# Kernel optimization log

Hardware: AMD Instinct MI355X
Metric: run time of the kernel (lower is better)

## Reference

```python
import jax, jax.numpy as jnp
import numpy as np

B, T, C, U = 64, 250, 1024, 512


def setup_inputs() -> dict:
    key = jax.random.key(0)
    ks = jax.random.split(key, 9)
    inputs = jax.random.normal(ks[0], (B, T, C), dtype=jnp.float32)
    # contiguous padding mask: True for valid positions
    seq_len = jax.random.randint(ks[1], (B,), T // 2, T + 1)
    mask = jnp.arange(T)[None, :] < seq_len[:, None]
    s_in = 1.0 / np.sqrt(C)
    s_rec = 1.0 / np.sqrt(U)
    Wf = jax.random.normal(ks[2], (C, 3 * U), dtype=jnp.float32) * s_in
    Uf = jax.random.normal(ks[3], (U, 3 * U), dtype=jnp.float32) * s_rec
    bf = jnp.zeros((2, 3 * U), dtype=jnp.float32)  # [input_bias, recurrent_bias] (reset_after=True)
    Wb = jax.random.normal(ks[4], (C, 3 * U), dtype=jnp.float32) * s_in
    Ub = jax.random.normal(ks[5], (U, 3 * U), dtype=jnp.float32) * s_rec
    bb = jnp.zeros((2, 3 * U), dtype=jnp.float32)
    return {"inputs": inputs, "mask": mask, "Wf": Wf, "Uf": Uf, "bf": bf,
            "Wb": Wb, "Ub": Ub, "bb": bb}


def _gru(x_tbc, m_tb, W, Uk, b):
    """Keras GRU v2 (reset_after=True) with masking. x_tbc: [T,B,C], m_tb: [T,B]."""
    # precompute input projections for all timesteps: [T,B,3U]
    xg = jnp.einsum('tbc,cg->tbg', x_tbc, W) + b[0]

    def step(h, inp):
        xg_t, m_t = inp
        hg = h @ Uk + b[1]  # [B,3U]
        xz, xr, xh = jnp.split(xg_t, 3, axis=-1)
        hz, hr, hh = jnp.split(hg, 3, axis=-1)
        z = jax.nn.sigmoid(xz + hz)
        r = jax.nn.sigmoid(xr + hr)
        c = jnp.tanh(xh + r * hh)
        h_new = z * h + (1.0 - z) * c
        h_new = jnp.where(m_t[:, None], h_new, h)  # carry state through masked steps
        return h_new, h_new

    h0 = jnp.zeros((x_tbc.shape[1], Uk.shape[0]), x_tbc.dtype)
    hT, ys = jax.lax.scan(step, h0, (xg, m_tb))
    return ys, hT  # ys: [T,B,U], hT: [B,U]


def reference(inputs, mask, Wf, Uf, bf, Wb, Ub, bb):
    x_t = jnp.transpose(inputs, (1, 0, 2))  # [T,B,C]
    m_t = mask.T  # [T,B]
    y_f, h_f = _gru(x_t, m_t, Wf, Uf, bf)
    # go_backwards: process reversed sequence, then reverse outputs back
    y_b, h_b = _gru(x_t[::-1], m_t[::-1], Wb, Ub, bb)
    y_b = y_b[::-1]
    seq_out = jnp.transpose(jnp.concatenate([y_f, y_b], axis=-1), (1, 0, 2))  # [B,T,2U]
    state_out = jnp.concatenate([h_f, h_b], axis=-1)  # [B,2U]
    return seq_out, state_out
```

## Files before the change

### kernel.cpp

```cpp
#include <hip/hip_runtime.h>
#include <cmath>

#define BB 64
#define TT 250
#define CC 1024
#define GG 1536

typedef unsigned long long u64t;
typedef unsigned int uint32;
typedef unsigned short ushort16;
typedef __attribute__((ext_vector_type(8))) short short8v;
typedef __attribute__((ext_vector_type(4))) float f32x4;

#define O_XGF 0
#define O_XGB 24576000
#define O_UT  49152000
#define O_MF  50724864
#define O_VH  50740864
#define O_WT  51003008

__device__ __forceinline__ unsigned short f2bf(float f) {
  unsigned u = __float_as_uint(f);
  return (unsigned short)((u + 0x7fffu + ((u >> 16) & 1u)) >> 16);
}
__device__ __forceinline__ float bf2f(unsigned short h) {
  return __uint_as_float((unsigned)h << 16);
}
__device__ __forceinline__ void cvt2(float a, float b, uint32& hi, uint32& lo) {
  unsigned short ha = f2bf(a), hb = f2bf(b);
  hi = (uint32)ha | ((uint32)hb << 16);
  lo = (uint32)f2bf(a - bf2f(ha)) | ((uint32)f2bf(b - bf2f(hb)) << 16);
}

__global__ __launch_bounds__(256) void prep_kernel(
    const unsigned char* __restrict__ mraw,
    float* __restrict__ ut, float* __restrict__ mf, u64t* __restrict__ vh,
    const float* __restrict__ Uf, const float* __restrict__ Ub)
{
  int idx = blockIdx.x * 256 + threadIdx.x;
  if (idx < 2*512*3*512) {
    int k = idx & 511;
    int r = idx >> 9;
    int g = r % 3;
    int rest = r / 3;
    int u = rest & 511;
    int dd = rest >> 9;
    const float* Um = dd ? Ub : Uf;
    ut[idx] = Um[k*GG + (g << 9) + u];
  }
  if (idx < 131072)
    __hip_atomic_store(&vh[idx], 0ULL, __ATOMIC_RELAXED, __HIP_MEMORY_SCOPE_AGENT);
  if (idx < BB*TT) {
    int b = idx / TT, t = idx - b*TT;
    bool bytefmt = (mraw[1] == 1);
    bool mv = bytefmt ? (mraw[idx] != 0) : (((const int*)mraw)[idx] != 0);
    mf[t*BB + b] = mv ? 1.0f : 0.0f;
  }
}

__global__ __launch_bounds__(256) void wt_build(
    const float* __restrict__ Wf, const float* __restrict__ Wb,
    ushort16* __restrict__ wt_hi, ushort16* __restrict__ wt_lo)
{
  __shared__ float tile[64][65];
  const int k0 = blockIdx.x * 64;
  const int n0 = blockIdx.y * 64;
  const int d  = blockIdx.z;
  const float* W = d ? Wb : Wf;
  const int l = threadIdx.x & 63, w = threadIdx.x >> 6;
  #pragma unroll
  for (int j = 0; j < 16; j++) {
    int r = j*4 + w;
    tile[r][l] = W[(size_t)(k0+r)*GG + n0 + l];
  }
  __syncthreads();
  #pragma unroll
  for (int j = 0; j < 16; j++) {
    int r = j*4 + w;
    float f = tile[l][r];
    unsigned short h = f2bf(f);
    size_t o = (size_t)(d*GG + n0 + r)*1024 + k0 + l;
    wt_hi[o] = h;
    wt_lo[o] = f2bf(f - bf2f(h));
  }
}

#define LDFRAG(dst, arr, row, kg) do { \
    union { uint4 u; short8v s; } r_; \
    r_.u = *(const uint4*)&arr[(row)*40 + ((kg) << 3)]; \
    dst = r_.s; } while (0)

__global__ __launch_bounds__(256) void gemm_xg(
    const float* __restrict__ A,
    const ushort16* __restrict__ wt_hi, const ushort16* __restrict__ wt_lo,
    const float* __restrict__ bf, const float* __restrict__ bb,
    float* __restrict__ xgf, float* __restrict__ xgb)
{
  __shared__ __align__(16) ushort16 Ah[128*40];
  __shared__ __align__(16) ushort16 Al[128*40];
  __shared__ __align__(16) ushort16 Bh[128*40];
  __shared__ __align__(16) ushort16 Bl[128*40];
  const int tid = threadIdx.x;
  const int l  = tid & 63;
  const int wv = tid >> 6;
  const int wm = wv & 1;
  const int wn = wv >> 1;
  const int t0 = blockIdx.x * 2;
  const int n0 = blockIdx.y * 128;
  const int d  = (n0 >= GG) ? 1 : 0;
  const int nl0 = n0 - d*GG;
  const float* bias = d ? bb : bf;
  float* xg = d ? xgb : xgf;

  const int sr = tid >> 1;
  const int sk = (tid & 1) << 4;
  const ushort16* whp = wt_hi + (size_t)(d*GG + nl0 + sr)*1024 + sk;
  const ushort16* wlp = wt_lo + (size_t)(d*GG + nl0 + sr)*1024 + sk;
  const int mrow = (sr & 63)*TT + t0 + (sr >> 6);
  const float* xp = A + (size_t)mrow*CC + sk;

  f32x4 acc[4][4];
  #pragma unroll
  for (int i = 0; i < 4; i++)
    #pragma unroll
    for (int j = 0; j < 4; j++) acc[i][j] = (f32x4){0.f,0.f,0.f,0.f};

  const int kg = l >> 4;
  for (int k0 = 0; k0 < CC; k0 += 32) {
    uint4 ha = *(const uint4*)(whp + k0);
    uint4 hb = *(const uint4*)(whp + k0 + 8);
    uint4 la = *(const uint4*)(wlp + k0);
    uint4 lb = *(const uint4*)(wlp + k0 + 8);
    float4 x0 = *(const float4*)(xp + k0);
    float4 x1 = *(const float4*)(xp + k0 + 4);
    float4 x2 = *(const float4*)(xp + k0 + 8);
    float4 x3 = *(const float4*)(xp + k0 + 12);
    __syncthreads();
    {
      *(uint4*)&Ah[sr*40 + sk]     = ha;
      *(uint4*)&Ah[sr*40 + sk + 8] = hb;
      *(uint4*)&Al[sr*40 + sk]     = la;
      *(uint4*)&Al[sr*40 + sk + 8] = lb;
      uint32 bhv[8], blv[8];
      cvt2(x0.x, x0.y, bhv[0], blv[0]); cvt2(x0.z, x0.w, bhv[1], blv[1]);
      cvt2(x1.x, x1.y, bhv[2], blv[2]); cvt2(x1.z, x1.w, bhv[3], blv[3]);
      cvt2(x2.x, x2.y, bhv[4], blv[4]); cvt2(x2.z, x2.w, bhv[5], blv[5]);
      cvt2(x3.x, x3.y, bhv[6], blv[6]); cvt2(x3.z, x3.w, bhv[7], blv[7]);
      *(uint4*)&Bh[sr*40 + sk]     = make_uint4(bhv[0], bhv[1], bhv[2], bhv[3]);
      *(uint4*)&Bh[sr*40 + sk + 8] = make_uint4(bhv[4], bhv[5], bhv[6], bhv[7]);
      *(uint4*)&Bl[sr*40 + sk]     = make_uint4(blv[0], blv[1], blv[2], blv[3]);
      *(uint4*)&Bl[sr*40 + sk + 8] = make_uint4(blv[4], blv[5], blv[6], blv[7]);
    }
    __syncthreads();
    short8v afh[4], afl[4], bfh[4], bfl[4];
    #pragma unroll
    for (int i = 0; i < 4; i++) {
      const int rA = wn*64 + i*16 + (l & 15);
      LDFRAG(afh[i], Ah, rA, kg);
      LDFRAG(afl[i], Al, rA, kg);
      const int rB = wm*64 + i*16 + (l & 15);
      LDFRAG(bfh[i], Bh, rB, kg);
      LDFRAG(bfl[i], Bl, rB, kg);
    }
    #pragma unroll
    for (int i = 0; i < 4; i++)
      #pragma unroll
      for (int j = 0; j < 4; j++) {
        acc[i][j] = __builtin_amdgcn_mfma_f32_16x16x32_bf16(afh[i], bfh[j], acc[i][j], 0, 0, 0);
        acc[i][j] = __builtin_amdgcn_mfma_f32_16x16x32_bf16(afh[i], bfl[j], acc[i][j], 0, 0, 0);
        acc[i][j] = __builtin_amdgcn_mfma_f32_16x16x32_bf16(afl[i], bfh[j], acc[i][j], 0, 0, 0);
      }
  }
  const int t = t0 + wm;
  #pragma unroll
  for (int i = 0; i < 4; i++) {
    const int ugl = wn*64 + i*16 + ((l >> 4) << 2);
    #pragma unroll
    for (int r = 0; r < 4; r++) {
      const int n = nl0 + ugl + r;
      const float bv = bias[n];
      float* orow = xg + (size_t)t*98304 + ((size_t)(n >> 9) << 15) + ((n & 511) << 6);
      #pragma unroll
      for (int j = 0; j < 4; j++)
        orow[j*16 + (l & 15)] = acc[i][j][r] + bv;
    }
  }
}

__global__ __launch_bounds__(512, 2) void gru_scan(
    float* xgf, float* xgb,
    const float* __restrict__ ut, const float* __restrict__ bf,
    const float* __restrict__ bb, const float* __restrict__ mf,
    u64t* vh, float* __restrict__ out)
{
  __shared__ __align__(16) unsigned short Bhi[8192];
  __shared__ __align__(16) unsigned short Blo[8192];
  const int tid = threadIdx.x;
  const int l   = tid & 63;
  const int wv  = tid >> 6;
  const int bid = blockIdx.x;
  const int d     = bid >> 6;
  const int mb    = (bid >> 2) & 15;
  const int btile = bid & 3;

  short8v af_hi[16], af_lo[16];
  {
    const int row = (wv << 4) | (l & 15);
    const int g   = row & 3;
    const int ua  = (mb << 5) | (row >> 2);
    const int kg_ = (l >> 4) << 3;
    if (g < 3) {
      const float* ap = ut + (((size_t)(((d << 9) | ua) * 3 + g)) << 9);
      #pragma unroll
      for (int ks = 0; ks < 16; ks++) {
        #pragma unroll
        for (int j = 0; j < 8; j++) {
          float f = ap[(ks << 5) + kg_ + j];
          unsigned short h = f2bf(f);
          af_hi[ks][j] = (short)h;
          af_lo[ks][j] = (short)f2bf(f - bf2f(h));
        }
      }
    } else {
      #pragma unroll
      for (int ks = 0; ks < 16; ks++)
        #pragma unroll
        for (int j = 0; j < 8; j++) { af_hi[ks][j] = 0; af_lo[ks][j] = 0; }
    }
  }

  const int u  = (mb << 5) | (wv << 2) | (l >> 4);
  const int b  = (btile << 4) | (l & 15);
  const float* bias = (d ? bb : bf) + GG;
  const float b1z = bias[u], b1r = bias[512+u], b1h = bias[1024+u];
  float* xg = d ? xgb : xgf;
  float hprev = 0.0f;

  const int kc  = tid >> 4;
  const int blw = tid & 15;
  const int cb  = (btile << 4) | blw;
  const int ksub_w = kc >> 1;
  const int qbase  = (kc & 1) << 1;
  const int boff = ((l & 15) << 6) + (((l >> 4) ^ ((l >> 1) & 3)) << 4);

  const int tf = d ? (TT-1) : 0;
  const float* xp0 = xg + (size_t)tf*98304 + (u << 6) + b;
  float xz = xp0[0], xr = xp0[32768], xh = xp0[65536];
  float m = mf[tf*BB + b];

  for (int s = 0; s < TT; s++) {
    const unsigned us_ = (unsigned)s;
    const int t = d ? (TT-1-s) : s;
    u64t* vin = vh + (size_t)((((unsigned)s & 1u) << 1) | (unsigned)d) * 32768;

    u64t v[16];
    #pragma unroll
    for (int i = 0; i < 16; i++)
      v[i] = __hip_atomic_load(vin + ((kc << 4) + i)*64 + cb, __ATOMIC_RELAXED, __HIP_MEMORY_SCOPE_AGENT);
    while (true) {
      int bad = 0;
      #pragma unroll
      for (int i = 0; i < 16; i++) bad |= ((unsigned)(v[i] >> 32) < us_) ? 1 : 0;
      if (!__any(bad)) break;
      __builtin_amdgcn_s_sleep(1);
      #pragma unroll
      for (int i = 0; i < 16; i++)
        if ((unsigned)(v[i] >> 32) < us_)
          v[i] = __hip_atomic_load(vin + ((kc << 4) + i)*64 + cb, __ATOMIC_RELAXED, __HIP_MEMORY_SCOPE_AGENT);
    }

    __syncthreads();
    #pragma unroll
    for (int half = 0; half < 2; half++) {
      uint32 hw[4], lw[4];
      #pragma unroll
      for (int p = 0; p < 4; p++) {
        u64t v0 = v[(half << 3) + (p << 1)];
        u64t v1 = v[(half << 3) + (p << 1) + 1];
        hw[p] = (uint32)((v0 >> 16) & 0xffffu) | ((uint32)((v1 >> 16) & 0xffffu) << 16);
        lw[p] = (uint32)(v0 & 0xffffu)         | ((uint32)(v1 & 0xffffu) << 16);
      }
      const int phys = (qbase + half) ^ ((blw >> 1) & 3);
      const int off = (ksub_w << 10) + (blw << 6) + (phys << 4);
      *(uint4*)((char*)Bhi + off) = make_uint4(hw[0], hw[1], hw[2], hw[3]);
      *(uint4*)((char*)Blo + off) = make_uint4(lw[0], lw[1], lw[2], lw[3]);
    }
    __syncthreads();

    float xz_n = 0.f, xr_n = 0.f, xh_n = 0.f, m_n = 0.f;
    if (s+1 < TT) {
      const int t2 = d ? (TT-2-s) : (s+1);
      const float* xp = xg + (size_t)t2*98304 + (u << 6) + b;
      xz_n = xp[0]; xr_n = xp[32768]; xh_n = xp[65536];
      m_n  = mf[t2*BB + b];
    }

    f32x4 acc0 = {0.f,0.f,0.f,0.f};
    f32x4 acc1 = {0.f,0.f,0.f,0.f};
    f32x4 acc2 = {0.f,0.f,0.f,0.f};
    #pragma unroll
    for (int ks = 0; ks < 16; ks++) {
      short8v bh  = *(const short8v*)((const char*)Bhi + (ks << 10) + boff);
      short8v bl8 = *(const short8v*)((const char*)Blo + (ks << 10) + boff);
      acc0 = __builtin_amdgcn_mfma_f32_16x16x32_bf16(af_hi[ks], bh,  acc0, 0, 0, 0);
      acc1 = __builtin_amdgcn_mfma_f32_16x16x32_bf16(af_hi[ks], bl8, acc1, 0, 0, 0);
      acc2 = __builtin_amdgcn_mfma_f32_16x16x32_bf16(af_lo[ks], bh,  acc2, 0, 0, 0);
    }
    float az = acc0[0] + acc1[0] + acc2[0];
    float ar = acc0[1] + acc1[1] + acc2[1];
    float ah = acc0[2] + acc1[2] + acc2[2];

    float z  = 1.0f / (1.0f + expf(-(xz + az + b1z)));
    float r  = 1.0f / (1.0f + expf(-(xr + ar + b1r)));
    float cc = tanhf(xh + r * (ah + b1h));
    float hn = z*hprev + (1.0f - z)*cc;
    hn = (m != 0.0f) ? hn : hprev;
    hprev = hn;

    u64t* vout = vh + (size_t)(((((unsigned)s + 1u) & 1u) << 1) | (unsigned)d) * 32768;
    unsigned short hh = f2bf(hn);
    unsigned short hl = f2bf(hn - bf2f(hh));
    u64t pk = ((u64t)(unsigned)(s+1) << 32) | ((u64t)hh << 16) | (u64t)hl;
    __hip_atomic_store(&vout[(u << 6) | b], pk, __ATOMIC_RELAXED, __HIP_MEMORY_SCOPE_AGENT);
    xg[(size_t)t*98304 + ((size_t)u << 6) + b] = hn;
    xz = xz_n; xr = xr_n; xh = xh_n; m = m_n;
  }
  out[16384000ull + ((size_t)b << 10) + (d << 9) + u] = hprev;
}

__global__ __launch_bounds__(256) void y_transpose(
    const float* __restrict__ xgf, const float* __restrict__ xgb,
    float* __restrict__ out)
{
  __shared__ float tile[64][65];
  const int t  = blockIdx.x;
  const int ch = blockIdx.y;
  const int d  = ch >> 3, uc = ch & 7;
  const float* src = (d ? xgb : xgf) + (size_t)t*98304 + (size_t)uc*4096;
  const int lane = threadIdx.x & 63, w = threadIdx.x >> 6;
  #pragma unroll
  for (int j = 0; j < 16; j++) {
    int r = j*4 + w;
    tile[r][lane] = src[r*64 + lane];
  }
  __syncthreads();
  #pragma unroll
  for (int j = 0; j < 16; j++) {
    int b = j*4 + w;
    out[((size_t)b*TT + t)*1024 + (d << 9) + (uc << 6) + lane] = tile[lane][b];
  }
}

extern "C" void kernel_launch(void* const* d_in, const int* in_sizes, int n_in,
                              void* d_out, int out_size, void* d_ws, size_t ws_size,
                              hipStream_t stream) {
  const float* X  = (const float*)d_in[0];
  const unsigned char* Mk = (const unsigned char*)d_in[1];
  const float* Wf = (const float*)d_in[2];
  const float* Uf = (const float*)d_in[3];
  const float* bf = (const float*)d_in[4];
  const float* Wb = (const float*)d_in[5];
  const float* Ub = (const float*)d_in[6];
  const float* bb = (const float*)d_in[7];
  float* out = (float*)d_out;
  float* ws  = (float*)d_ws;
  float* xgf = ws + O_XGF;
  float* xgb = ws + O_XGB;
  float* ut  = ws + O_UT;
  float* mf  = ws + O_MF;
  u64t*  vh  = (u64t*)(ws + O_VH);
  ushort16* wt_hi = (ushort16*)(ws + O_WT);
  ushort16* wt_lo = wt_hi + (size_t)2*GG*1024;

  prep_kernel<<<dim3(6144), dim3(256), 0, stream>>>(Mk, ut, mf, vh, Uf, Ub);
  wt_build<<<dim3(16, 24, 2), dim3(256), 0, stream>>>(Wf, Wb, wt_hi, wt_lo);
  gemm_xg<<<dim3(125, 24), dim3(256), 0, stream>>>(X, wt_hi, wt_lo, bf, bb, xgf, xgb);
  gru_scan<<<dim3(128), dim3(512), 0, stream>>>(xgf, xgb, ut, bf, bb, mf, vh, out);
  y_transpose<<<dim3(TT, 16), dim3(256), 0, stream>>>(xgf, xgb, out);
}
```

Baseline: 1.549 ms.

## Replace per-element step tags with per-wave flags in GRU scan handoff

The hidden-state exchange between workgroups previously carried a 64-bit value per element with an embedded step counter, and each consumer polled all 16 loaded elements. Now the hidden state is stored as 32-bit hi/lo bf16 pairs, and each wave publishes one step flag after a vmcnt wait. Consumers spin on 128 flags per direction/batch tile before loading the data. This halves exchange traffic and shrinks the polling footprint, but relies on relaxed ordering plus s_waitcnt for visibility, which risks memory-ordering races.

```diff
diff --git a/kernel.cpp b/kernel.cpp
--- a/kernel.cpp
+++ b/kernel.cpp
@@ -17,6 +17,7 @@
 #define O_UT  49152000
 #define O_MF  50724864
 #define O_VH  50740864
+#define O_FL  50871936
 #define O_WT  51003008
 
 __device__ __forceinline__ unsigned short f2bf(float f) {
@@ -34,7 +35,8 @@
 
 __global__ __launch_bounds__(256) void prep_kernel(
     const unsigned char* __restrict__ mraw,
-    float* __restrict__ ut, float* __restrict__ mf, u64t* __restrict__ vh,
+    float* __restrict__ ut, float* __restrict__ mf,
+    uint32* __restrict__ vh2, uint32* __restrict__ fl,
     const float* __restrict__ Uf, const float* __restrict__ Ub)
 {
   int idx = blockIdx.x * 256 + threadIdx.x;
@@ -49,7 +51,9 @@
     ut[idx] = Um[k*GG + (g << 9) + u];
   }
   if (idx < 131072)
-    __hip_atomic_store(&vh[idx], 0ULL, __ATOMIC_RELAXED, __HIP_MEMORY_SCOPE_AGENT);
+    __hip_atomic_store(&vh2[idx], 0u, __ATOMIC_RELAXED, __HIP_MEMORY_SCOPE_AGENT);
+  if (idx < 1024)
+    __hip_atomic_store(&fl[idx], 0u, __ATOMIC_RELAXED, __HIP_MEMORY_SCOPE_AGENT);
   if (idx < BB*TT) {
     int b = idx / TT, t = idx - b*TT;
     bool bytefmt = (mraw[1] == 1);
@@ -191,7 +195,7 @@
     float* xgf, float* xgb,
     const float* __restrict__ ut, const float* __restrict__ bf,
     const float* __restrict__ bb, const float* __restrict__ mf,
-    u64t* vh, float* __restrict__ out)
+    uint32* vh2, uint32* fl, float* __restrict__ out)
 {
   __shared__ __align__(16) unsigned short Bhi[8192];
   __shared__ __align__(16) unsigned short Blo[8192];
@@ -243,6 +247,10 @@
   const int qbase  = (kc & 1) << 1;
   const int boff = ((l & 15) << 6) + (((l >> 4) ^ ((l >> 1) & 3)) << 4);
 
+  uint32* flg = fl + (((d << 2) | btile) << 7);
+  const u64t* flp = (const u64t*)flg;
+  uint32* myflag = flg + (mb << 3) + wv;
+
   const int tf = d ? (TT-1) : 0;
   const float* xp0 = xg + (size_t)tf*98304 + (u << 6) + b;
   float xz = xp0[0], xr = xp0[32768], xh = xp0[65536];
@@ -251,23 +259,19 @@
   for (int s = 0; s < TT; s++) {
     const unsigned us_ = (unsigned)s;
     const int t = d ? (TT-1-s) : s;
-    u64t* vin = vh + (size_t)((((unsigned)s & 1u) << 1) | (unsigned)d) * 32768;
-
-    u64t v[16];
+    uint32* vin = vh2 + (size_t)((((unsigned)s & 1u) << 1) | (unsigned)d) * 32768;
+
+    while (true) {
+      u64t fv = __hip_atomic_load(&flp[l], __ATOMIC_RELAXED, __HIP_MEMORY_SCOPE_AGENT);
+      if (__all(((unsigned)fv >= us_) && ((unsigned)(fv >> 32) >= us_))) break;
+      __builtin_amdgcn_s_sleep(1);
+    }
+    asm volatile("" ::: "memory");
+
+    uint32 v[16];
     #pragma unroll
     for (int i = 0; i < 16; i++)
       v[i] = __hip_atomic_load(vin + ((kc << 4) + i)*64 + cb, __ATOMIC_RELAXED, __HIP_MEMORY_SCOPE_AGENT);
-    while (true) {
-      int bad = 0;
-      #pragma unroll
-      for (int i = 0; i < 16; i++) bad |= ((unsigned)(v[i] >> 32) < us_) ? 1 : 0;
-      if (!__any(bad)) break;
-      __builtin_amdgcn_s_sleep(1);
-      #pragma unroll
-      for (int i = 0; i < 16; i++)
-        if ((unsigned)(v[i] >> 32) < us_)
-          v[i] = __hip_atomic_load(vin + ((kc << 4) + i)*64 + cb, __ATOMIC_RELAXED, __HIP_MEMORY_SCOPE_AGENT);
-    }
 
     __syncthreads();
     #pragma unroll
@@ -275,10 +279,10 @@
       uint32 hw[4], lw[4];
       #pragma unroll
       for (int p = 0; p < 4; p++) {
-        u64t v0 = v[(half << 3) + (p << 1)];
-        u64t v1 = v[(half << 3) + (p << 1) + 1];
-        hw[p] = (uint32)((v0 >> 16) & 0xffffu) | ((uint32)((v1 >> 16) & 0xffffu) << 16);
-        lw[p] = (uint32)(v0 & 0xffffu)         | ((uint32)(v1 & 0xffffu) << 16);
+        uint32 v0 = v[(half << 3) + (p << 1)];
+        uint32 v1 = v[(half << 3) + (p << 1) + 1];
+        hw[p] = (v0 >> 16) | (v1 & 0xffff0000u);
+        lw[p] = (v0 & 0xffffu) | (v1 << 16);
       }
       const int phys = (qbase + half) ^ ((blw >> 1) & 3);
       const int off = (ksub_w << 10) + (blw << 6) + (phys << 4);
@@ -317,11 +321,14 @@
     hn = (m != 0.0f) ? hn : hprev;
     hprev = hn;
 
-    u64t* vout = vh + (size_t)(((((unsigned)s + 1u) & 1u) << 1) | (unsigned)d) * 32768;
+    uint32* vout = vh2 + (size_t)(((((unsigned)s + 1u) & 1u) << 1) | (unsigned)d) * 32768;
     unsigned short hh = f2bf(hn);
     unsigned short hl = f2bf(hn - bf2f(hh));
-    u64t pk = ((u64t)(unsigned)(s+1) << 32) | ((u64t)hh << 16) | (u64t)hl;
+    uint32 pk = ((uint32)hh << 16) | (uint32)hl;
     __hip_atomic_store(&vout[(u << 6) | b], pk, __ATOMIC_RELAXED, __HIP_MEMORY_SCOPE_AGENT);
+    asm volatile("s_waitcnt vmcnt(0)" ::: "memory");
+    if (l == 0)
+      __hip_atomic_store(myflag, (uint32)(s + 1), __ATOMIC_RELAXED, __HIP_MEMORY_SCOPE_AGENT);
     xg[(size_t)t*98304 + ((size_t)u << 6) + b] = hn;
     xz = xz_n; xr = xr_n; xh = xh_n; m = m_n;
   }
@@ -368,13 +375,14 @@
   float* xgb = ws + O_XGB;
   float* ut  = ws + O_UT;
   float* mf  = ws + O_MF;
-  u64t*  vh  = (u64t*)(ws + O_VH);
+  uint32* vh2 = (uint32*)(ws + O_VH);
+  uint32* fl  = (uint32*)(ws + O_FL);
   ushort16* wt_hi = (ushort16*)(ws + O_WT);
   ushort16* wt_lo = wt_hi + (size_t)2*GG*1024;
 
-  prep_kernel<<<dim3(6144), dim3(256), 0, stream>>>(Mk, ut, mf, vh, Uf, Ub);
+  prep_kernel<<<dim3(6144), dim3(256), 0, stream>>>(Mk, ut, mf, vh2, fl, Uf, Ub);
   wt_build<<<dim3(16, 24, 2), dim3(256), 0, stream>>>(Wf, Wb, wt_hi, wt_lo);
   gemm_xg<<<dim3(125, 24), dim3(256), 0, stream>>>(X, wt_hi, wt_lo, bf, bb, xgf, xgb);
-  gru_scan<<<dim3(128), dim3(512), 0, stream>>>(xgf, xgb, ut, bf, bb, mf, vh, out);
+  gru_scan<<<dim3(128), dim3(512), 0, stream>>>(xgf, xgb, ut, bf, bb, mf, vh2, fl, out);
   y_transpose<<<dim3(TT, 16), dim3(256), 0, stream>>>(xgf, xgb, out);
 }
```

Result: slower. 2.210 ms (+42.7%).

## Double-buffer scan LDS, deepen xg prefetch, and tile the recurrent-weight transpose

Applied to the files above, without the earlier changes.

The recurrent scan kernel now alternates between two LDS buffers for the hidden-state operands, so the first __syncthreads per step can be dropped. It also prefetches the input-gate values two timesteps ahead instead of one, and skips the sleep on the first failed poll of the spin-wait. The Uf/Ub transpose moves out of the strided prep kernel into a shared-memory tiled kernel with coalesced reads and writes. Together these aim to cut per-step latency in the serial recurrence and speed up setup, at the cost of twice the LDS, more registers, and a busier poll loop.

```diff
diff --git a/kernel.cpp b/kernel.cpp
--- a/kernel.cpp
+++ b/kernel.cpp
@@ -32,22 +32,11 @@
   lo = (uint32)f2bf(a - bf2f(ha)) | ((uint32)f2bf(b - bf2f(hb)) << 16);
 }
 
-__global__ __launch_bounds__(256) void prep_kernel(
+__global__ __launch_bounds__(256) void prep_small(
     const unsigned char* __restrict__ mraw,
-    float* __restrict__ ut, float* __restrict__ mf, u64t* __restrict__ vh,
-    const float* __restrict__ Uf, const float* __restrict__ Ub)
+    float* __restrict__ mf, u64t* __restrict__ vh)
 {
   int idx = blockIdx.x * 256 + threadIdx.x;
-  if (idx < 2*512*3*512) {
-    int k = idx & 511;
-    int r = idx >> 9;
-    int g = r % 3;
-    int rest = r / 3;
-    int u = rest & 511;
-    int dd = rest >> 9;
-    const float* Um = dd ? Ub : Uf;
-    ut[idx] = Um[k*GG + (g << 9) + u];
-  }
   if (idx < 131072)
     __hip_atomic_store(&vh[idx], 0ULL, __ATOMIC_RELAXED, __HIP_MEMORY_SCOPE_AGENT);
   if (idx < BB*TT) {
@@ -55,6 +44,30 @@
     bool bytefmt = (mraw[1] == 1);
     bool mv = bytefmt ? (mraw[idx] != 0) : (((const int*)mraw)[idx] != 0);
     mf[t*BB + b] = mv ? 1.0f : 0.0f;
+  }
+}
+
+__global__ __launch_bounds__(256) void ut_build(
+    const float* __restrict__ Uf, const float* __restrict__ Ub,
+    float* __restrict__ ut)
+{
+  __shared__ float tile[64][65];
+  const int k0 = blockIdx.x * 64;
+  const int n0 = blockIdx.y * 64;
+  const int d  = blockIdx.z;
+  const float* Um = d ? Ub : Uf;
+  const int l = threadIdx.x & 63, w = threadIdx.x >> 6;
+  #pragma unroll
+  for (int j = 0; j < 16; j++) {
+    int r = j*4 + w;
+    tile[r][l] = Um[(size_t)(k0+r)*GG + n0 + l];
+  }
+  __syncthreads();
+  #pragma unroll
+  for (int j = 0; j < 16; j++) {
+    int r = j*4 + w;
+    int n = n0 + r, u = n & 511, g = n >> 9;
+    ut[(size_t)(((d << 9) | u)*3 + g)*512 + k0 + l] = tile[l][r];
   }
 }
 
@@ -193,8 +206,8 @@
     const float* __restrict__ bb, const float* __restrict__ mf,
     u64t* vh, float* __restrict__ out)
 {
-  __shared__ __align__(16) unsigned short Bhi[8192];
-  __shared__ __align__(16) unsigned short Blo[8192];
+  __shared__ __align__(16) unsigned short Bhi[2][8192];
+  __shared__ __align__(16) unsigned short Blo[2][8192];
   const int tid = threadIdx.x;
   const int l   = tid & 63;
   const int wv  = tid >> 6;
@@ -243,10 +256,15 @@
   const int qbase  = (kc & 1) << 1;
   const int boff = ((l & 15) << 6) + (((l >> 4) ^ ((l >> 1) & 3)) << 4);
 
-  const int tf = d ? (TT-1) : 0;
-  const float* xp0 = xg + (size_t)tf*98304 + (u << 6) + b;
-  float xz = xp0[0], xr = xp0[32768], xh = xp0[65536];
-  float m = mf[tf*BB + b];
+  float xzA, xrA, xhA, mA, xzB, xrB, xhB, mB;
+  {
+    const int tA = d ? (TT-1) : 0;
+    const float* p = xg + (size_t)tA*98304 + (u << 6) + b;
+    xzA = p[0]; xrA = p[32768]; xhA = p[65536]; mA = mf[tA*BB + b];
+    const int tB = d ? (TT-2) : 1;
+    const float* q = xg + (size_t)tB*98304 + (u << 6) + b;
+    xzB = q[0]; xrB = q[32768]; xhB = q[65536]; mB = mf[tB*BB + b];
+  }
 
   for (int s = 0; s < TT; s++) {
     const unsigned us_ = (unsigned)s;
@@ -257,19 +275,22 @@
     #pragma unroll
     for (int i = 0; i < 16; i++)
       v[i] = __hip_atomic_load(vin + ((kc << 4) + i)*64 + cb, __ATOMIC_RELAXED, __HIP_MEMORY_SCOPE_AGENT);
+    int slept = 0;
     while (true) {
       int bad = 0;
       #pragma unroll
       for (int i = 0; i < 16; i++) bad |= ((unsigned)(v[i] >> 32) < us_) ? 1 : 0;
       if (!__any(bad)) break;
-      __builtin_amdgcn_s_sleep(1);
+      if (slept) __builtin_amdgcn_s_sleep(1);
+      slept = 1;
       #pragma unroll
       for (int i = 0; i < 16; i++)
         if ((unsigned)(v[i] >> 32) < us_)
           v[i] = __hip_atomic_load(vin + ((kc << 4) + i)*64 + cb, __ATOMIC_RELAXED, __HIP_MEMORY_SCOPE_AGENT);
     }
 
-    __syncthreads();
+    unsigned short* BhiS = Bhi[s & 1];
+    unsigned short* BloS = Blo[s & 1];
     #pragma unroll
     for (int half = 0; half < 2; half++) {
       uint32 hw[4], lw[4];
@@ -282,17 +303,17 @@
       }
       const int phys = (qbase + half) ^ ((blw >> 1) & 3);
       const int off = (ksub_w << 10) + (blw << 6) + (phys << 4);
-      *(uint4*)((char*)Bhi + off) = make_uint4(hw[0], hw[1], hw[2], hw[3]);
-      *(uint4*)((char*)Blo + off) = make_uint4(lw[0], lw[1], lw[2], lw[3]);
+      *(uint4*)((char*)BhiS + off) = make_uint4(hw[0], hw[1], hw[2], hw[3]);
+      *(uint4*)((char*)BloS + off) = make_uint4(lw[0], lw[1], lw[2], lw[3]);
     }
     __syncthreads();
 
-    float xz_n = 0.f, xr_n = 0.f, xh_n = 0.f, m_n = 0.f;
-    if (s+1 < TT) {
-      const int t2 = d ? (TT-2-s) : (s+1);
+    float xzC = 0.f, xrC = 0.f, xhC = 0.f, mC = 0.f;
+    if (s+2 < TT) {
+      const int t2 = d ? (TT-3-s) : (s+2);
       const float* xp = xg + (size_t)t2*98304 + (u << 6) + b;
-      xz_n = xp[0]; xr_n = xp[32768]; xh_n = xp[65536];
-      m_n  = mf[t2*BB + b];
+      xzC = xp[0]; xrC = xp[32768]; xhC = xp[65536];
+      mC  = mf[t2*BB + b];
     }
 
     f32x4 acc0 = {0.f,0.f,0.f,0.f};
@@ -300,8 +321,8 @@
     f32x4 acc2 = {0.f,0.f,0.f,0.f};
     #pragma unroll
     for (int ks = 0; ks < 16; ks++) {
-      short8v bh  = *(const short8v*)((const char*)Bhi + (ks << 10) + boff);
-      short8v bl8 = *(const short8v*)((const char*)Blo + (ks << 10) + boff);
+      short8v bh  = *(const short8v*)((const char*)BhiS + (ks << 10) + boff);
+      short8v bl8 = *(const short8v*)((const char*)BloS + (ks << 10) + boff);
       acc0 = __builtin_amdgcn_mfma_f32_16x16x32_bf16(af_hi[ks], bh,  acc0, 0, 0, 0);
       acc1 = __builtin_amdgcn_mfma_f32_16x16x32_bf16(af_hi[ks], bl8, acc1, 0, 0, 0);
       acc2 = __builtin_amdgcn_mfma_f32_16x16x32_bf16(af_lo[ks], bh,  acc2, 0, 0, 0);
@@ -310,11 +331,11 @@
     float ar = acc0[1] + acc1[1] + acc2[1];
     float ah = acc0[2] + acc1[2] + acc2[2];
 
-    float z  = 1.0f / (1.0f + expf(-(xz + az + b1z)));
-    float r  = 1.0f / (1.0f + expf(-(xr + ar + b1r)));
-    float cc = tanhf(xh + r * (ah + b1h));
+    float z  = 1.0f / (1.0f + expf(-(xzA + az + b1z)));
+    float r  = 1.0f / (1.0f + expf(-(xrA + ar + b1r)));
+    float cc = tanhf(xhA + r * (ah + b1h));
     float hn = z*hprev + (1.0f - z)*cc;
-    hn = (m != 0.0f) ? hn : hprev;
+    hn = (mA != 0.0f) ? hn : hprev;
     hprev = hn;
 
     u64t* vout = vh + (size_t)(((((unsigned)s + 1u) & 1u) << 1) | (unsigned)d) * 32768;
@@ -323,7 +344,8 @@
     u64t pk = ((u64t)(unsigned)(s+1) << 32) | ((u64t)hh << 16) | (u64t)hl;
     __hip_atomic_store(&vout[(u << 6) | b], pk, __ATOMIC_RELAXED, __HIP_MEMORY_SCOPE_AGENT);
     xg[(size_t)t*98304 + ((size_t)u << 6) + b] = hn;
-    xz = xz_n; xr = xr_n; xh = xh_n; m = m_n;
+    xzA = xzB; xrA = xrB; xhA = xhB; mA = mB;
+    xzB = xzC; xrB = xrC; xhB = xhC; mB = mC;
   }
   out[16384000ull + ((size_t)b << 10) + (d << 9) + u] = hprev;
 }
@@ -372,7 +394,8 @@
   ushort16* wt_hi = (ushort16*)(ws + O_WT);
   ushort16* wt_lo = wt_hi + (size_t)2*GG*1024;
 
-  prep_kernel<<<dim3(6144), dim3(256), 0, stream>>>(Mk, ut, mf, vh, Uf, Ub);
+  prep_small<<<dim3(512), dim3(256), 0, stream>>>(Mk, mf, vh);
+  ut_build<<<dim3(8, 24, 2), dim3(256), 0, stream>>>(Uf, Ub, ut);
   wt_build<<<dim3(16, 24, 2), dim3(256), 0, stream>>>(Wf, Wb, wt_hi, wt_lo);
   gemm_xg<<<dim3(125, 24), dim3(256), 0, stream>>>(X, wt_hi, wt_lo, bf, bb, xgf, xgb);
   gru_scan<<<dim3(128), dim3(512), 0, stream>>>(xgf, xgb, ut, bf, bb, mf, vh, out);
```

Measured after the change: 1.522 ms. About the same (-1.7%).
